# Kernel tuning notes

Measured on AMD Instinct MI355X. Metric: run time of the kernel, lower is better.

## Reference

```python
import jax, jax.numpy as jnp
import numpy as np

K = 16          # num clusters
DZ = 64         # dim_zt == dim_zi (required by decoder matmul)
DT = 1024       # treatment feature dim (dim_t)
NT = 2048       # number of treatments == dim_x (columns of input_ins)
NI = 4096       # number of instances
MU_P_WT = 5.0
COS_EPS = 1e-6


def setup_inputs() -> dict:
    key = jax.random.key(0)
    ks = jax.random.split(key, 12)
    s = 0.02
    return {
        "input_ins": jax.random.uniform(ks[0], (NI, NT), dtype=jnp.float32),
        "input_treat": jax.random.normal(ks[1], (NT, DT), dtype=jnp.float32),
        # nn.Linear params (torch layout: W [out, in], y = x @ W.T + b)
        "W_mu_zt": jax.random.normal(ks[2], (DZ, DT)) * s,
        "b_mu_zt": jnp.zeros((DZ,), jnp.float32),
        "W_lv_zt": jax.random.normal(ks[3], (DZ, DT)) * s,
        "b_lv_zt": jnp.zeros((DZ,), jnp.float32),
        "W_arec": jax.random.normal(ks[4], (DT, DZ)) * s,
        "b_arec": jnp.zeros((DT,), jnp.float32),
        "W_mu_zi": jax.random.normal(ks[5], (DZ, NT)) * s,
        "b_mu_zi": jnp.zeros((DZ,), jnp.float32),
        "W_lv_zi": jax.random.normal(ks[6], (DZ, NT)) * s,
        "b_lv_zi": jnp.zeros((DZ,), jnp.float32),
        "mu_p_zt": jax.random.normal(ks[7], (K, DZ), dtype=jnp.float32),
        "logvar_p_zt": jnp.ones((K, DZ), jnp.float32),
        "W_y1": jax.random.normal(ks[8], (K * DZ, DZ)) * s,
        "b_y1": jnp.zeros((K * DZ,), jnp.float32),
        "W_y2": jax.random.normal(ks[9], (1, K * DZ)) * s,
        "b_y2": jnp.zeros((1,), jnp.float32),
    }


def reference(input_ins, input_treat, W_mu_zt, b_mu_zt, W_lv_zt, b_lv_zt,
              W_arec, b_arec, W_mu_zi, b_mu_zi, W_lv_zi, b_lv_zi,
              mu_p_zt, logvar_p_zt, W_y1, b_y1, W_y2, b_y2):
    # encode_t (eval mode: zt_sample = mu_zt)
    mu_zt = input_treat @ W_mu_zt.T + b_mu_zt           # [NT, DZ]
    logvar_zt = input_treat @ W_lv_zt.T + b_lv_zt       # [NT, DZ]
    zt = mu_zt

    # compute_qc (cosine similarity vs scaled cluster centers, *10)
    centers = MU_P_WT * mu_p_zt                          # [K, DZ]
    num = zt @ centers.T                                 # [NT, K]
    denom = jnp.maximum(
        jnp.linalg.norm(zt, axis=1, keepdims=True) * jnp.linalg.norm(centers, axis=1)[None, :],
        COS_EPS)
    qc_raw = 10.0 * num / denom                          # [NT, K]
    cates = jax.nn.softmax(qc_raw, axis=1)               # forward softmaxes qc once
    c_sample = jax.nn.softmax(cates, axis=1)             # encode_i (eval) softmaxes again

    # encode_i, vectorized over K clusters: (input_ins * cates_k) @ W.T + b
    # fused einsum avoids materializing the [K, NI, NT] masked inputs
    mu_zi = jnp.einsum('nt,tk,dt->knd', input_ins, c_sample, W_mu_zi) + b_mu_zi       # [K, NI, DZ]
    logvar_zi = jnp.einsum('nt,tk,dt->knd', input_ins, c_sample, W_lv_zi) + b_lv_zi   # [K, NI, DZ]
    zi = mu_zi  # eval-mode reparameterize

    # a_reconstby_zt
    a_reconst = jax.nn.sigmoid(zt @ W_arec.T + b_arec)   # [NT, DT]

    # decoder: sum_k sigmoid(zi_k @ zt.T) * cates_k
    logits = jnp.einsum('knd,td->knt', zi, zt)           # [K, NI, NT]
    a_pred = jnp.einsum('knt,tk->nt', jax.nn.sigmoid(logits), c_sample)  # [NI, NT]

    # predictY
    zi_all = jnp.transpose(zi, (1, 0, 2)).reshape(zi.shape[1], K * DZ)   # cat over k, dim=1
    a_zt = input_ins @ zt                                # [NI, DZ]
    rep_w1 = a_zt @ W_y1.T + b_y1                        # [NI, K*DZ]
    pred_y2 = zi_all @ W_y2.T + b_y2                     # [NI, 1]
    # diag(rep_w1 @ zi_all.T) == rowwise dot product (no NIxNI matmul)
    mu_y = jnp.sum(rep_w1 * zi_all, axis=1, keepdims=True) + pred_y2     # [NI, 1]
    logvar_y = jnp.ones_like(mu_y)

    return (mu_zt, logvar_zt, mu_p_zt, logvar_p_zt, cates, mu_zi, logvar_zi,
            zi, a_pred, mu_y, logvar_y, a_reconst)
```

## Files before the change

### kernel.cpp

```cpp
#include <hip/hip_runtime.h>

typedef unsigned short ushort_t;
typedef unsigned int   uint32;
typedef __attribute__((ext_vector_type(8))) short short8;
typedef __attribute__((ext_vector_type(4))) float f32x4;

#define DEV __device__ __forceinline__

#define KC 16
#define DZ 64
#define DT 1024
#define NT 2048
#define NI 4096
#define KD 1024

#define O_MU_ZT   0
#define O_LV_ZT   131072
#define O_MU_P    262144
#define O_LV_P    263168
#define O_CATES   264192
#define O_MU_ZI   296960
#define O_LV_ZI   4491264
#define O_ZI      8685568
#define O_APRED   12879872
#define O_MU_Y    21268480
#define O_LV_Y    21272576
#define O_AREC    21276672

#define WSF_ZT   0
#define WSF_C    131072
#define WSF_CT   163840
#define WSF_AZT  196608
#define WSF_END  458752
#define WSU_ZTB  0
#define WSU_BC   131072
#define WSU_ZIB  4325376
#define WSU_INSB 8519680
#define WSU_ZHT  16908288
#define WSU_ZLT  17039360

DEV ushort_t f2b(float f){
  uint32 u = __float_as_uint(f);
  u += 0x7fffu + ((u >> 16) & 1u);
  return (ushort_t)(u >> 16);
}
DEV uint32 pk(float lo, float hi){
  return (__float_as_uint(hi) & 0xffff0000u) | (__float_as_uint(lo) >> 16);
}
DEV float wred64(float v){
#pragma unroll
  for (int m = 32; m; m >>= 1) v += __shfl_xor(v, m, 64);
  return v;
}
DEV float fastrcp(float x){ return __builtin_amdgcn_rcpf(x); }
DEV void gl2lds16(ushort_t* l, const ushort_t* g){
  __builtin_amdgcn_global_load_lds(
      (const __attribute__((address_space(1))) unsigned int*)g,
      (__attribute__((address_space(3))) unsigned int*)l, 16, 0, 0);
}

__global__ __launch_bounds__(256) void k_encode_t(
    const float* __restrict__ treat, const float* __restrict__ Wmu,
    const float* __restrict__ bmu, const float* __restrict__ Wlv,
    const float* __restrict__ blv, float* __restrict__ out,
    float* __restrict__ ws_zt)
{
  __shared__ float rowsh[8 * DT];
  const int n0 = blockIdx.x * 8, tid = threadIdx.x;
  const float4* src = (const float4*)(treat + (size_t)n0 * DT);
#pragma unroll
  for (int i = 0; i < 8; ++i)
    ((float4*)rowsh)[tid + i * 256] = src[tid + i * 256];
  __syncthreads();
  const int j = tid & 127, half = tid >> 7;
  const bool isMu = j < 64;
  const int jj = j & 63;
  const float* W = (isMu ? Wmu : Wlv) + (size_t)jj * DT;
  const float bias = isMu ? bmu[jj] : blv[jj];
  float a0 = bias, a1 = bias, a2 = bias, a3 = bias;
  const float4* w4 = (const float4*)W;
  const float4* r0 = (const float4*)&rowsh[(half*4 + 0) * DT];
  const float4* r1 = (const float4*)&rowsh[(half*4 + 1) * DT];
  const float4* r2 = (const float4*)&rowsh[(half*4 + 2) * DT];
  const float4* r3 = (const float4*)&rowsh[(half*4 + 3) * DT];
#pragma unroll 4
  for (int i = 0; i < DT / 4; ++i){
    float4 wv = w4[i];
    float4 v0 = r0[i], v1 = r1[i], v2 = r2[i], v3 = r3[i];
    a0 += wv.x*v0.x + wv.y*v0.y + wv.z*v0.z + wv.w*v0.w;
    a1 += wv.x*v1.x + wv.y*v1.y + wv.z*v1.z + wv.w*v1.w;
    a2 += wv.x*v2.x + wv.y*v2.y + wv.z*v2.z + wv.w*v2.w;
    a3 += wv.x*v3.x + wv.y*v3.y + wv.z*v3.z + wv.w*v3.w;
  }
  float acc[4] = {a0, a1, a2, a3};
#pragma unroll
  for (int r = 0; r < 4; ++r){
    const int row = n0 + half*4 + r;
    if (isMu){ out[O_MU_ZT + row*DZ + jj] = acc[r]; ws_zt[row*DZ + jj] = acc[r]; }
    else     { out[O_LV_ZT + row*DZ + jj] = acc[r]; }
  }
}

__global__ __launch_bounds__(256) void k_qc(
    const float* __restrict__ mu_p, const float* __restrict__ ws_zt,
    float* __restrict__ out, float* __restrict__ ws_c, float* __restrict__ ws_cT)
{
  const int tid = threadIdx.x, lane = tid & 63;
  const int row = blockIdx.x * 4 + (tid >> 6);
  const float z = ws_zt[row * DZ + lane];
  const float nz = sqrtf(wred64(z * z));
  float myqc = 0.f;
#pragma unroll
  for (int k = 0; k < KC; ++k){
    float cv  = 5.f * mu_p[k * DZ + lane];
    float dot = wred64(z * cv);
    float nc2 = wred64(cv * cv);
    float qc  = 10.f * dot / fmaxf(nz * sqrtf(nc2), 1e-6f);
    if (lane == k) myqc = qc;
  }
  float mx = myqc;
#pragma unroll
  for (int m = 8; m; m >>= 1) mx = fmaxf(mx, __shfl_xor(mx, m, 16));
  float e = __expf(myqc - mx);
  float s = e;
#pragma unroll
  for (int m = 8; m; m >>= 1) s += __shfl_xor(s, m, 16);
  float cates = e / s;
  float mx2 = cates;
#pragma unroll
  for (int m = 8; m; m >>= 1) mx2 = fmaxf(mx2, __shfl_xor(mx2, m, 16));
  float e2 = __expf(cates - mx2);
  float s2 = e2;
#pragma unroll
  for (int m = 8; m; m >>= 1) s2 += __shfl_xor(s2, m, 16);
  float c2 = e2 / s2;
  if (lane < KC){
    out[O_CATES + row * KC + lane] = cates;
    ws_c[row * KC + lane] = c2;
    ws_cT[lane * NT + row] = c2;
  }
}

__global__ __launch_bounds__(256) void k_prep(
    const float* __restrict__ Wmu, const float* __restrict__ Wlv,
    const float* __restrict__ cT, const float* __restrict__ zt,
    const float* __restrict__ ins,
    ushort_t* __restrict__ Bc, ushort_t* __restrict__ ztb,
    ushort_t* __restrict__ insb,
    ushort_t* __restrict__ zhT, ushort_t* __restrict__ zlT,
    const float* __restrict__ mu_p, const float* __restrict__ lv_p,
    float* __restrict__ out)
{
  const int bx = blockIdx.x, tid = threadIdx.x;
  if (bx < 2048){
    const int j = bx;
    const bool isMu = j < KD;
    const int kk = (j & (KD-1)) >> 6, d = j & 63;
    const float* W = (isMu ? Wmu : Wlv) + (size_t)d * NT;
    const float* c = cT + (size_t)kk * NT;
    const int t = tid * 8;
    float4 w0 = *(const float4*)(W + t), w1 = *(const float4*)(W + t + 4);
    float4 c0 = *(const float4*)(c + t), c1 = *(const float4*)(c + t + 4);
    ushort_t v[8];
    v[0]=f2b(w0.x*c0.x); v[1]=f2b(w0.y*c0.y); v[2]=f2b(w0.z*c0.z); v[3]=f2b(w0.w*c0.w);
    v[4]=f2b(w1.x*c1.x); v[5]=f2b(w1.y*c1.y); v[6]=f2b(w1.z*c1.z); v[7]=f2b(w1.w*c1.w);
    *(uint4*)(Bc + (size_t)j * NT + t) = *(uint4*)v;
  } else if (bx < 2080){
    const int g = (bx - 2048) * 256 + tid;
    const int base = g * 16;
    const float4* src = (const float4*)(zt + base);
    float4 z0 = src[0], z1 = src[1], z2 = src[2], z3 = src[3];
    ushort_t v[16];
    v[0]=f2b(z0.x); v[1]=f2b(z0.y); v[2]=f2b(z0.z); v[3]=f2b(z0.w);
    v[4]=f2b(z1.x); v[5]=f2b(z1.y); v[6]=f2b(z1.z); v[7]=f2b(z1.w);
    v[8]=f2b(z2.x); v[9]=f2b(z2.y); v[10]=f2b(z2.z); v[11]=f2b(z2.w);
    v[12]=f2b(z3.x); v[13]=f2b(z3.y); v[14]=f2b(z3.z); v[15]=f2b(z3.w);
    *(uint4*)(ztb + base) = *(uint4*)&v[0];
    *(uint4*)(ztb + base + 8) = *(uint4*)&v[8];
  } else if (bx < 2084){
    const int i = (bx - 2080) * 256 + tid;
    out[O_MU_P + i] = mu_p[i];
    out[O_LV_P + i] = lv_p[i];
  } else if (bx < 4132){
    const int g = (bx - 2084) * 256 + tid;
    const int base = g * 16;
    const float4* src = (const float4*)(ins + base);
    float4 z0 = src[0], z1 = src[1], z2 = src[2], z3 = src[3];
    ushort_t v[16];
    v[0]=f2b(z0.x); v[1]=f2b(z0.y); v[2]=f2b(z0.z); v[3]=f2b(z0.w);
    v[4]=f2b(z1.x); v[5]=f2b(z1.y); v[6]=f2b(z1.z); v[7]=f2b(z1.w);
    v[8]=f2b(z2.x); v[9]=f2b(z2.y); v[10]=f2b(z2.z); v[11]=f2b(z2.w);
    v[12]=f2b(z3.x); v[13]=f2b(z3.y); v[14]=f2b(z3.z); v[15]=f2b(z3.w);
    *(uint4*)(insb + base) = *(uint4*)&v[0];
    *(uint4*)(insb + base + 8) = *(uint4*)&v[8];
  } else {
    __shared__ float zsh[64 * 65];
    const int t0 = (bx - 4132) * 64;
#pragma unroll
    for (int jj = 0; jj < 16; ++jj){
      const int idx = jj * 256 + tid;
      const int t = idx >> 6, d = idx & 63;
      zsh[t * 65 + d] = zt[(size_t)(t0 + t) * DZ + d];
    }
    __syncthreads();
    const int d = tid >> 2, tq = tid & 3;
    ushort_t vh[16], vl[16];
#pragma unroll
    for (int i = 0; i < 16; ++i){
      const float f = zsh[(tq * 16 + i) * 65 + d];
      const uint32 u = __float_as_uint(f);
      vh[i] = (ushort_t)(u >> 16);
      const float hf = __uint_as_float(u & 0xffff0000u);
      vl[i] = (ushort_t)(__float_as_uint(f - hf) >> 16);
    }
    *(uint4*)(zhT + (size_t)d * NT + t0 + tq * 16)     = *(uint4*)&vh[0];
    *(uint4*)(zhT + (size_t)d * NT + t0 + tq * 16 + 8) = *(uint4*)&vh[8];
    *(uint4*)(zlT + (size_t)d * NT + t0 + tq * 16)     = *(uint4*)&vl[0];
    *(uint4*)(zlT + (size_t)d * NT + t0 + tq * 16 + 8) = *(uint4*)&vl[8];
  }
}

__global__ __launch_bounds__(256) void k_encode_i(
    const ushort_t* __restrict__ insb, const ushort_t* __restrict__ Bc,
    const float* __restrict__ bmu, const float* __restrict__ blv,
    float* __restrict__ out, ushort_t* __restrict__ zib)
{
  __shared__ ushort_t As[128*64];
  __shared__ ushort_t Bs[128*64];
  const int tid = threadIdx.x;
  const int j0 = blockIdx.x * 128, n0 = blockIdx.y * 128;
  const int w = tid >> 6, lane = tid & 63;
  const int wm = w & 1, wn = w >> 1;
  const int l16 = lane & 15, quad = lane >> 4;

  const int srow = tid >> 3, schunk = (tid & 7) ^ (srow & 7);
  const ushort_t* aSrc = insb + (size_t)(n0 + srow) * NT + schunk * 8;
  const ushort_t* bSrc = Bc  + (size_t)(j0 + srow) * NT + schunk * 8;
  ushort_t* aDst = &As[tid * 8];
  ushort_t* bDst = &Bs[tid * 8];

  f32x4 acc[4][4] = {};

  for (int kt = 0; kt < NT/64; ++kt){
    const ushort_t* ak = aSrc + kt * 64;
    const ushort_t* bk = bSrc + kt * 64;
#pragma unroll
    for (int i = 0; i < 4; ++i){
      gl2lds16(aDst + i * 2048, ak + (size_t)i * 32 * NT);
      gl2lds16(bDst + i * 2048, bk + (size_t)i * 32 * NT);
    }
    __syncthreads();
#pragma unroll
    for (int ks = 0; ks < 2; ++ks){
      const int rsw = ((ks*4 + quad) ^ (l16 & 7)) * 8;
      short8 af[4], bf[4];
#pragma unroll
      for (int mf = 0; mf < 4; ++mf)
        af[mf] = *(const short8*)&As[(wm*64 + mf*16 + l16)*64 + rsw];
#pragma unroll
      for (int nf = 0; nf < 4; ++nf)
        bf[nf] = *(const short8*)&Bs[(wn*64 + nf*16 + l16)*64 + rsw];
#pragma unroll
      for (int mf = 0; mf < 4; ++mf)
#pragma unroll
        for (int nf = 0; nf < 4; ++nf)
          acc[mf][nf] = __builtin_amdgcn_mfma_f32_16x16x32_bf16(af[mf], bf[nf], acc[mf][nf], 0, 0, 0);
    }
    __syncthreads();
  }

  const int colW = j0 + wn * 64;
  const bool isMu = colW < KD;
  const int kk = (colW & (KD - 1)) >> 6;
  const float* bias = isMu ? bmu : blv;
  const size_t zbase = (size_t)kk * (NI * DZ);
#pragma unroll
  for (int mf = 0; mf < 4; ++mf){
    const int r = n0 + wm*64 + mf*16 + quad*4;
#pragma unroll
    for (int nf = 0; nf < 4; ++nf){
      const int d = nf*16 + l16;
      const float bv = bias[d];
#pragma unroll
      for (int reg = 0; reg < 4; ++reg){
        float v = acc[mf][nf][reg] + bv;
        size_t idx = zbase + (size_t)(r + reg)*DZ + d;
        if (isMu){
          out[O_MU_ZI + idx] = v;
          out[O_ZI + idx] = v;
          zib[idx] = f2b(v);
        } else {
          out[O_LV_ZI + idx] = v;
        }
      }
    }
  }
}

__global__ __launch_bounds__(256) void k_decoder(
    const ushort_t* __restrict__ ztb, const ushort_t* __restrict__ zib,
    const float* __restrict__ ws_c, float* __restrict__ out)
{
  __shared__ ushort_t Zt[64*64];
  __shared__ ushort_t Zi[128*64];
  __shared__ float ct[64*17];
  const int tid = threadIdx.x;
  const int t0 = blockIdx.x * 64, n0 = blockIdx.y * 128;
  const int w = tid >> 6, lane = tid & 63;
  const int wm = w & 1, wn = w >> 1;
  const int l16 = lane & 15, quad = lane >> 4;
  const int zr = tid >> 2, zq = tid & 3;
  const int ir = tid >> 1, ih = tid & 1;
  {
    const uint4* src = (const uint4*)(ztb + (size_t)(t0 + zr)*DZ + zq*16);
    uint4 z0 = src[0], z1 = src[1];
    ushort_t* dst = &Zt[zr*64];
    *(uint4*)&dst[((zq*2 + 0) ^ (zr & 7)) * 8] = z0;
    *(uint4*)&dst[((zq*2 + 1) ^ (zr & 7)) * 8] = z1;
  }
  for (int i = tid; i < 64*16; i += 256){
    int t = i >> 4, k = i & 15;
    ct[t*17 + k] = ws_c[(size_t)(t0 + t)*KC + k];
  }
  const ushort_t* iG = zib + (size_t)(n0 + ir)*DZ + ih*32;
  ushort_t* isw = &Zi[ir*64];
  const int sw0 = ((ih*4 + 0) ^ (ir & 7)) * 8;
  const int sw1 = ((ih*4 + 1) ^ (ir & 7)) * 8;
  const int sw2 = ((ih*4 + 2) ^ (ir & 7)) * 8;
  const int sw3 = ((ih*4 + 3) ^ (ir & 7)) * 8;
  uint4 Zr0, Zr1, Zr2, Zr3;
  {
    const uint4* zp = (const uint4*)iG;
    Zr0 = zp[0]; Zr1 = zp[1]; Zr2 = zp[2]; Zr3 = zp[3];
  }
  f32x4 accum[4][2] = {};
  for (int k = 0; k < KC; ++k){
    __syncthreads();
    *(uint4*)&isw[sw0] = Zr0; *(uint4*)&isw[sw1] = Zr1;
    *(uint4*)&isw[sw2] = Zr2; *(uint4*)&isw[sw3] = Zr3;
    __syncthreads();
    if (k < KC - 1){
      const uint4* zp = (const uint4*)(iG + (size_t)(k+1)*(NI*DZ));
      Zr0 = zp[0]; Zr1 = zp[1]; Zr2 = zp[2]; Zr3 = zp[3];
    }
    f32x4 s[4][2] = {};
#pragma unroll
    for (int ks = 0; ks < 2; ++ks){
      const int rsw = ((ks*4 + quad) ^ (l16 & 7)) * 8;
      short8 af[4], bf[2];
#pragma unroll
      for (int mf = 0; mf < 4; ++mf)
        af[mf] = *(const short8*)&Zi[(wm*64 + mf*16 + l16)*64 + rsw];
#pragma unroll
      for (int nf = 0; nf < 2; ++nf)
        bf[nf] = *(const short8*)&Zt[(wn*32 + nf*16 + l16)*64 + rsw];
#pragma unroll
      for (int mf = 0; mf < 4; ++mf)
#pragma unroll
        for (int nf = 0; nf < 2; ++nf)
          s[mf][nf] = __builtin_amdgcn_mfma_f32_16x16x32_bf16(af[mf], bf[nf], s[mf][nf], 0, 0, 0);
    }
#pragma unroll
    for (int nf = 0; nf < 2; ++nf){
      const float cv = ct[(wn*32 + nf*16 + l16)*17 + k];
#pragma unroll
      for (int mf = 0; mf < 4; ++mf)
#pragma unroll
        for (int reg = 0; reg < 4; ++reg)
          accum[mf][nf][reg] += cv * fastrcp(1.f + __expf(-s[mf][nf][reg]));
    }
  }
#pragma unroll
  for (int mf = 0; mf < 4; ++mf){
    const int r = n0 + wm*64 + mf*16 + quad*4;
#pragma unroll
    for (int nf = 0; nf < 2; ++nf){
      const int col = t0 + wn*32 + nf*16 + l16;
#pragma unroll
      for (int reg = 0; reg < 4; ++reg)
        out[O_APRED + (size_t)(r + reg)*NT + col] = accum[mf][nf][reg];
    }
  }
}

__global__ __launch_bounds__(256) void k_arec(
    const float* __restrict__ ws_zt, const float* __restrict__ W,
    const float* __restrict__ bias, float* __restrict__ out)
{
  __shared__ float zsh[8 * DZ];
  const int n0 = blockIdx.x * 8, tid = threadIdx.x;
  if (tid < 128)
    ((float4*)zsh)[tid] = ((const float4*)(ws_zt + (size_t)n0 * DZ))[tid];
  __syncthreads();
#pragma unroll
  for (int jo = 0; jo < 4; ++jo){
    const int j = jo*256 + tid;
    const float4* w4 = (const float4*)(W + (size_t)j * DZ);
    const float b = bias[j];
    float acc[8];
#pragma unroll
    for (int r = 0; r < 8; ++r) acc[r] = b;
#pragma unroll
    for (int i = 0; i < 16; ++i){
      float4 wv = w4[i];
#pragma unroll
      for (int r = 0; r < 8; ++r){
        const float* z = &zsh[r*DZ + i*4];
        acc[r] += wv.x*z[0] + wv.y*z[1] + wv.z*z[2] + wv.w*z[3];
      }
    }
#pragma unroll
    for (int r = 0; r < 8; ++r)
      out[O_AREC + (size_t)(n0 + r)*DT + j] = fastrcp(1.f + __expf(-acc[r]));
  }
}

__global__ __launch_bounds__(256) void k_azt(
    const float* __restrict__ ins, const ushort_t* __restrict__ zhT,
    const ushort_t* __restrict__ zlT, float* __restrict__ azt)
{
  const int tid = threadIdx.x;
  const int n0 = blockIdx.x * 16;
  const int w = tid >> 6, lane = tid & 63;
  const int l16 = lane & 15, quad = lane >> 4;
  const float* aRow = ins + (size_t)(n0 + l16) * NT + quad * 8;
  const ushort_t* bh = zhT + (size_t)(w * 16 + l16) * NT + quad * 8;
  const ushort_t* bl = zlT + (size_t)(w * 16 + l16) * NT + quad * 8;
  f32x4 acc = {};
#pragma unroll 4
  for (int kt = 0; kt < 32; ++kt){
#pragma unroll
    for (int ks = 0; ks < 2; ++ks){
      const int ko = kt * 64 + ks * 32;
      float4 a0 = *(const float4*)(aRow + ko);
      float4 a1 = *(const float4*)(aRow + ko + 4);
      uint32 u0 = __float_as_uint(a0.x), u1 = __float_as_uint(a0.y);
      uint32 u2 = __float_as_uint(a0.z), u3 = __float_as_uint(a0.w);
      uint32 u4 = __float_as_uint(a1.x), u5 = __float_as_uint(a1.y);
      uint32 u6 = __float_as_uint(a1.z), u7 = __float_as_uint(a1.w);
      uint4 H, L;
      H.x = (u1 & 0xffff0000u) | (u0 >> 16);
      H.y = (u3 & 0xffff0000u) | (u2 >> 16);
      H.z = (u5 & 0xffff0000u) | (u4 >> 16);
      H.w = (u7 & 0xffff0000u) | (u6 >> 16);
      float l0 = a0.x - __uint_as_float(u0 & 0xffff0000u);
      float l1 = a0.y - __uint_as_float(u1 & 0xffff0000u);
      float l2 = a0.z - __uint_as_float(u2 & 0xffff0000u);
      float l3 = a0.w - __uint_as_float(u3 & 0xffff0000u);
      float l4 = a1.x - __uint_as_float(u4 & 0xffff0000u);
      float l5 = a1.y - __uint_as_float(u5 & 0xffff0000u);
      float l6 = a1.z - __uint_as_float(u6 & 0xffff0000u);
      float l7 = a1.w - __uint_as_float(u7 & 0xffff0000u);
      L.x = pk(l0, l1); L.y = pk(l2, l3); L.z = pk(l4, l5); L.w = pk(l6, l7);
      short8 ah = *(short8*)&H, al = *(short8*)&L;
      short8 bh8 = *(const short8*)(bh + ko);
      short8 bl8 = *(const short8*)(bl + ko);
      acc = __builtin_amdgcn_mfma_f32_16x16x32_bf16(ah, bh8, acc, 0, 0, 0);
      acc = __builtin_amdgcn_mfma_f32_16x16x32_bf16(al, bh8, acc, 0, 0, 0);
      acc = __builtin_amdgcn_mfma_f32_16x16x32_bf16(ah, bl8, acc, 0, 0, 0);
    }
  }
  const int col = w * 16 + l16;
#pragma unroll
  for (int reg = 0; reg < 4; ++reg)
    azt[(size_t)(n0 + quad * 4 + reg) * DZ + col] = acc[reg];
}

__global__ __launch_bounds__(256) void k_muy(
    const float* __restrict__ azt, const float* __restrict__ Wy1,
    const float* __restrict__ by1, const float* __restrict__ Wy2,
    const float* __restrict__ by2, const float* __restrict__ zi_out,
    float* __restrict__ out)
{
  __shared__ float sazt[16][DZ];
  const int tid = threadIdx.x;
  const int n0 = blockIdx.x * 16;
  for (int i = tid; i < 16*DZ; i += 256)
    sazt[i >> 6][i & 63] = azt[(size_t)(n0 + (i >> 6))*DZ + (i & 63)];
  __syncthreads();
  const int w = tid >> 6, lane = tid & 63;
  float s0 = 0.f, s1 = 0.f, s2 = 0.f, s3 = 0.f;
  for (int jj = 0; jj < 16; ++jj){
    const int j = jj*64 + lane;
    const float4* wr = (const float4*)(Wy1 + (size_t)j * DZ);
    float d0 = 0.f, d1 = 0.f, d2 = 0.f, d3 = 0.f;
    const float* a0 = sazt[w*4 + 0];
    const float* a1 = sazt[w*4 + 1];
    const float* a2 = sazt[w*4 + 2];
    const float* a3 = sazt[w*4 + 3];
#pragma unroll
    for (int i = 0; i < 16; ++i){
      float4 wv = wr[i];
      d0 += wv.x*a0[i*4] + wv.y*a0[i*4+1] + wv.z*a0[i*4+2] + wv.w*a0[i*4+3];
      d1 += wv.x*a1[i*4] + wv.y*a1[i*4+1] + wv.z*a1[i*4+2] + wv.w*a1[i*4+3];
      d2 += wv.x*a2[i*4] + wv.y*a2[i*4+1] + wv.z*a2[i*4+2] + wv.w*a2[i*4+3];
      d3 += wv.x*a3[i*4] + wv.y*a3[i*4+1] + wv.z*a3[i*4+2] + wv.w*a3[i*4+3];
    }
    const float add = by1[j] + Wy2[j];
    const size_t zb = (size_t)jj*(NI*DZ) + lane;
    s0 += (d0 + add) * zi_out[zb + (size_t)(n0 + w*4 + 0)*DZ];
    s1 += (d1 + add) * zi_out[zb + (size_t)(n0 + w*4 + 1)*DZ];
    s2 += (d2 + add) * zi_out[zb + (size_t)(n0 + w*4 + 2)*DZ];
    s3 += (d3 + add) * zi_out[zb + (size_t)(n0 + w*4 + 3)*DZ];
  }
  s0 = wred64(s0); s1 = wred64(s1); s2 = wred64(s2); s3 = wred64(s3);
  if (lane == 0){
    const float b = by2[0];
    out[O_MU_Y + n0 + w*4 + 0] = s0 + b;
    out[O_MU_Y + n0 + w*4 + 1] = s1 + b;
    out[O_MU_Y + n0 + w*4 + 2] = s2 + b;
    out[O_MU_Y + n0 + w*4 + 3] = s3 + b;
  }
  if (tid < 16) out[O_LV_Y + n0 + tid] = 1.0f;
}

extern "C" void kernel_launch(void* const* d_in, const int* in_sizes, int n_in,
                              void* d_out, int out_size, void* d_ws, size_t ws_size,
                              hipStream_t stream)
{
  (void)in_sizes; (void)n_in; (void)out_size; (void)ws_size;
  const float* ins   = (const float*)d_in[0];
  const float* treat = (const float*)d_in[1];
  const float* Wmzt  = (const float*)d_in[2];
  const float* bmzt  = (const float*)d_in[3];
  const float* Wlzt  = (const float*)d_in[4];
  const float* blzt  = (const float*)d_in[5];
  const float* Warec = (const float*)d_in[6];
  const float* barec = (const float*)d_in[7];
  const float* Wmzi  = (const float*)d_in[8];
  const float* bmzi  = (const float*)d_in[9];
  const float* Wlzi  = (const float*)d_in[10];
  const float* blzi  = (const float*)d_in[11];
  const float* mu_p  = (const float*)d_in[12];
  const float* lv_p  = (const float*)d_in[13];
  const float* Wy1   = (const float*)d_in[14];
  const float* by1   = (const float*)d_in[15];
  const float* Wy2   = (const float*)d_in[16];
  const float* by2   = (const float*)d_in[17];
  float* out = (float*)d_out;
  float* wsf = (float*)d_ws;
  ushort_t* wsu = (ushort_t*)(wsf + WSF_END);

  float* ws_zt  = wsf + WSF_ZT;
  float* ws_c   = wsf + WSF_C;
  float* ws_cT  = wsf + WSF_CT;
  float* ws_azt = wsf + WSF_AZT;
  ushort_t* ztb  = wsu + WSU_ZTB;
  ushort_t* Bc   = wsu + WSU_BC;
  ushort_t* zib  = wsu + WSU_ZIB;
  ushort_t* insb = wsu + WSU_INSB;
  ushort_t* zhT  = wsu + WSU_ZHT;
  ushort_t* zlT  = wsu + WSU_ZLT;

  k_encode_t<<<NT/8, 256, 0, stream>>>(treat, Wmzt, bmzt, Wlzt, blzt, out, ws_zt);
  k_qc      <<<NT/4, 256, 0, stream>>>(mu_p, ws_zt, out, ws_c, ws_cT);
  k_prep    <<<4164, 256, 0, stream>>>(Wmzi, Wlzi, ws_cT, ws_zt, ins, Bc, ztb, insb, zhT, zlT, mu_p, lv_p, out);
  k_encode_i<<<dim3(16, 32), 256, 0, stream>>>(insb, Bc, bmzi, blzi, out, zib);
  k_decoder <<<dim3(32, 32), 256, 0, stream>>>(ztb, zib, ws_c, out);
  k_arec    <<<NT/8, 256, 0, stream>>>(ws_zt, Warec, barec, out);
  k_azt     <<<NI/16, 256, 0, stream>>>(ins, zhT, zlT, ws_azt);
  k_muy     <<<NI/16, 256, 0, stream>>>(ws_azt, Wy1, by1, Wy2, by2, out + O_ZI, out);
}
```

Before: 420.2 us.

## Double-buffer LDS tiles in encode_i GEMM and swizzle block order

The k_encode_i GEMM now uses two LDS buffers, prefetching the next K-tile via global-to-LDS loads while MFMAs run on the current one, which drops one barrier per iteration. Block indices are remapped so consecutive blocks share operand tiles for better L2 reuse, and s_setprio raises wave priority around the MFMA burst. Doubling LDS to 64KB per block may cut occupancy. The single barrier per iteration depends on the async LDS loads being complete at that barrier.

New measurement: 413.6 us. No clear change (-1.6%).

```diff
diff --git a/kernel.cpp b/kernel.cpp
--- a/kernel.cpp
+++ b/kernel.cpp
@@ -225,10 +225,12 @@
     const float* __restrict__ bmu, const float* __restrict__ blv,
     float* __restrict__ out, ushort_t* __restrict__ zib)
 {
-  __shared__ ushort_t As[128*64];
-  __shared__ ushort_t Bs[128*64];
+  __shared__ ushort_t As[2*128*64];
+  __shared__ ushort_t Bs[2*128*64];
   const int tid = threadIdx.x;
-  const int j0 = blockIdx.x * 128, n0 = blockIdx.y * 128;
+  const int orig = blockIdx.y * 16 + blockIdx.x;
+  const int swz  = (orig & 7) * 64 + (orig >> 3);
+  const int j0 = (swz & 15) * 128, n0 = (swz >> 4) * 128;
   const int w = tid >> 6, lane = tid & 63;
   const int wm = w & 1, wn = w >> 1;
   const int l16 = lane & 15, quad = lane >> 4;
@@ -236,37 +238,51 @@
   const int srow = tid >> 3, schunk = (tid & 7) ^ (srow & 7);
   const ushort_t* aSrc = insb + (size_t)(n0 + srow) * NT + schunk * 8;
   const ushort_t* bSrc = Bc  + (size_t)(j0 + srow) * NT + schunk * 8;
-  ushort_t* aDst = &As[tid * 8];
-  ushort_t* bDst = &Bs[tid * 8];
 
   f32x4 acc[4][4] = {};
 
+#pragma unroll
+  for (int i = 0; i < 4; ++i){
+    gl2lds16(&As[tid*8] + i * 2048, aSrc + (size_t)i * 32 * NT);
+    gl2lds16(&Bs[tid*8] + i * 2048, bSrc + (size_t)i * 32 * NT);
+  }
+  __syncthreads();
+
+  int cur = 0;
   for (int kt = 0; kt < NT/64; ++kt){
-    const ushort_t* ak = aSrc + kt * 64;
-    const ushort_t* bk = bSrc + kt * 64;
-#pragma unroll
-    for (int i = 0; i < 4; ++i){
-      gl2lds16(aDst + i * 2048, ak + (size_t)i * 32 * NT);
-      gl2lds16(bDst + i * 2048, bk + (size_t)i * 32 * NT);
-    }
-    __syncthreads();
+    if (kt < NT/64 - 1){
+      const ushort_t* ak = aSrc + (kt+1) * 64;
+      const ushort_t* bk = bSrc + (kt+1) * 64;
+      ushort_t* ad = &As[(cur^1)*8192 + tid*8];
+      ushort_t* bd = &Bs[(cur^1)*8192 + tid*8];
+#pragma unroll
+      for (int i = 0; i < 4; ++i){
+        gl2lds16(ad + i * 2048, ak + (size_t)i * 32 * NT);
+        gl2lds16(bd + i * 2048, bk + (size_t)i * 32 * NT);
+      }
+    }
+    const ushort_t* Ab = &As[cur*8192];
+    const ushort_t* Bb = &Bs[cur*8192];
 #pragma unroll
     for (int ks = 0; ks < 2; ++ks){
       const int rsw = ((ks*4 + quad) ^ (l16 & 7)) * 8;
       short8 af[4], bf[4];
 #pragma unroll
       for (int mf = 0; mf < 4; ++mf)
-        af[mf] = *(const short8*)&As[(wm*64 + mf*16 + l16)*64 + rsw];
+        af[mf] = *(const short8*)&Ab[(wm*64 + mf*16 + l16)*64 + rsw];
 #pragma unroll
       for (int nf = 0; nf < 4; ++nf)
-        bf[nf] = *(const short8*)&Bs[(wn*64 + nf*16 + l16)*64 + rsw];
+        bf[nf] = *(const short8*)&Bb[(wn*64 + nf*16 + l16)*64 + rsw];
+      __builtin_amdgcn_s_setprio(1);
 #pragma unroll
       for (int mf = 0; mf < 4; ++mf)
 #pragma unroll
         for (int nf = 0; nf < 4; ++nf)
           acc[mf][nf] = __builtin_amdgcn_mfma_f32_16x16x32_bf16(af[mf], bf[nf], acc[mf][nf], 0, 0, 0);
+      __builtin_amdgcn_s_setprio(0);
     }
     __syncthreads();
+    cur ^= 1;
   }
 
   const int colW = j0 + wn * 64;
```
